# Kernel optimization log

Measured on AMD Instinct MI355X. Metric: run time of the kernel, lower is better.

Reference implementation:

```python
import jax, jax.numpy as jnp
import numpy as np

B, Q, KV = 8, 16, 2048
NQ, NK, NV, H = 512, 512, 512, 512

def setup_inputs() -> dict:
    key = jax.random.key(0)
    k = jax.random.split(key, 7)
    s = 0.02
    return {
        "query": jax.random.normal(k[0], (B, Q, NQ), jnp.float32),
        "keys": jax.random.normal(k[1], (B, KV, NK), jnp.float32),
        "values": jax.random.normal(k[2], (B, KV, NV), jnp.float32),
        "W_weight": jax.random.normal(k[3], (H, NQ + NK), jnp.float32) * s,
        "W_bias": jax.random.normal(k[4], (H,), jnp.float32) * s,
        "v_weight": jax.random.normal(k[5], (1, H), jnp.float32) * s,
        "v_bias": jax.random.normal(k[6], (1,), jnp.float32) * s,
    }

def reference(query, keys, values, W_weight, W_bias, v_weight, v_bias):
    # Split W over the concat axis: cat([query, keys]) @ W^T == query@Wq^T + keys@Wk^T
    Wq = W_weight[:, :NQ]   # [H, Nq]
    Wk = W_weight[:, NQ:]   # [H, Nk]
    q_part = jnp.einsum('bqn,hn->bqh', query, Wq)   # [B,Q,H]
    k_part = jnp.einsum('bkn,hn->bkh', keys, Wk)    # [B,KV,H]
    # broadcast-add -> [B,KV,Q,H], tanh, project to scalar energy
    energy = jnp.tanh(k_part[:, :, None, :] + q_part[:, None, :, :] + W_bias)
    e = jnp.einsum('bkqh,h->bkq', energy, v_weight[0]) + v_bias[0]  # [B,KV,Q]
    scores = jax.nn.softmax(e, axis=1)              # softmax over KV
    # output = (values^T @ scores)^T -> [B,Q,Nv]
    output = jnp.einsum('bkn,bkq->bqn', values, scores)
    return output
```

## Files before the change

### kernel.cpp

```cpp
#include <hip/hip_runtime.h>
#include <cstddef>

using bf16x8  = __attribute__((ext_vector_type(8))) short;
using short4v = __attribute__((ext_vector_type(4))) short;
using f32x4   = __attribute__((ext_vector_type(4))) float;
using ushort8 = __attribute__((ext_vector_type(8))) unsigned short;

#define GLL16(gp, lp) __builtin_amdgcn_global_load_lds( \
    (const __attribute__((address_space(1))) unsigned int*)(const void*)(gp), \
    (__attribute__((address_space(3))) unsigned int*)(void*)(lp), 16, 0, 0)

__device__ __forceinline__ float exp2_f(float x){ float r; asm("v_exp_f32 %0, %1" : "=v"(r) : "v"(x)); return r; }
__device__ __forceinline__ float rcp_f (float x){ float r; asm("v_rcp_f32 %0, %1" : "=v"(r) : "v"(x)); return r; }
__device__ __forceinline__ unsigned pk2(float lo, float hi){
  unsigned r; asm("v_cvt_pk_bf16_f32 %0, %1, %2" : "=v"(r) : "v"(lo), "v"(hi)); return r;
}
__device__ __forceinline__ unsigned short f2bf(float f){
  unsigned int u = __float_as_uint(f);
  u = u + 0x7FFFu + ((u >> 16) & 1u);
  return (unsigned short)(u >> 16);
}
__device__ __forceinline__ float bf2f(unsigned short s){
  return __uint_as_float(((unsigned int)s) << 16);
}

#define KEYS_N   8388608
#define WK_N     262144
#define CONV_BLOCKS 4224
#define SCALE_2LOG2E 2.885390081777927f

#define OFF_KEYS_BF   0u
#define OFF_WK_BF     16777216u
#define OFF_EQB       17301504u
#define OFF_EPART     17563648u
#define OFF_SC        21757952u

__global__ __launch_bounds__(256) void k_convert(
    const float* __restrict__ keys, const float* __restrict__ W,
    const float* __restrict__ query,
    unsigned short* __restrict__ keys_bf, unsigned short* __restrict__ wk_bf,
    float* __restrict__ eqb)
{
  __shared__ short qg[128*32 + 32*32];
  if (blockIdx.x >= CONV_BLOCKS) {
    const int nb = blockIdx.x - CONV_BLOCKS;
    const int n0 = nb * 32;
    const int tid = threadIdx.x;
    const int l = tid & 63, w = tid >> 6;
    short* A  = qg;
    short* Bs = qg + 4096;
    const int sub = tid >> 3;
    const int c4  = (tid & 7) * 4;
    const int wm = w & 1, wn = w >> 1;
    const int fr = l & 15, fg = l >> 4;

    f32x4 acc[4];
    #pragma unroll
    for (int i = 0; i < 4; ++i) acc[i] = (f32x4){0.f,0.f,0.f,0.f};

    for (int kt = 0; kt < 16; ++kt) {
      const int k0 = kt * 32;
      float4 a4[4];
      #pragma unroll
      for (int m = 0; m < 4; ++m)
        a4[m] = *(const float4*)(query + (size_t)(m * 32 + sub) * 512 + k0 + c4);
      const float4 b4 = *(const float4*)(W + (size_t)(n0 + sub) * 1024 + k0 + c4);
      __syncthreads();
      #pragma unroll
      for (int m = 0; m < 4; ++m) {
        const int row = m * 32 + sub;
        const int o = row * 32 + (((c4 >> 3) ^ ((row >> 1) & 3)) << 3) + (c4 & 7);
        *(uint2*)&A[o] = make_uint2(pk2(a4[m].x, a4[m].y), pk2(a4[m].z, a4[m].w));
      }
      {
        const int o = sub * 32 + (((c4 >> 3) ^ ((sub >> 1) & 3)) << 3) + (c4 & 7);
        *(uint2*)&Bs[o] = make_uint2(pk2(b4.x, b4.y), pk2(b4.z, b4.w));
      }
      __syncthreads();
      bf16x8 af[4], bfv;
      #pragma unroll
      for (int i = 0; i < 4; ++i) {
        const int ar = wm*64 + i*16 + fr;
        af[i] = *(const bf16x8*)&A[ar*32 + ((fg ^ ((ar>>1)&3)) << 3)];
      }
      const int br = wn*16 + fr;
      bfv = *(const bf16x8*)&Bs[br*32 + ((fg ^ ((br>>1)&3)) << 3)];
      #pragma unroll
      for (int i = 0; i < 4; ++i)
        acc[i] = __builtin_amdgcn_mfma_f32_16x16x32_bf16(af[i], bfv, acc[i], 0, 0, 0);
    }
    const int gh = n0 + wn*16 + fr;
    #pragma unroll
    for (int i = 0; i < 4; ++i)
      #pragma unroll
      for (int r = 0; r < 4; ++r) {
        const int gm = wm*64 + i*16 + fg*4 + r;
        eqb[gm * 512 + gh] = exp2_f(acc[i][r] * SCALE_2LOG2E);
      }
    return;
  }
  int idx = (blockIdx.x * 256 + threadIdx.x) * 8;
  const float* src;
  unsigned short* dst;
  if (idx < KEYS_N) { src = keys + idx; dst = keys_bf + idx; }
  else {
    int e = idx - KEYS_N;
    src = W + (size_t)(e >> 9) * 1024 + 512 + (e & 511);
    dst = wk_bf + e;
  }
  float4 a = *(const float4*)src;
  float4 b = *(const float4*)(src + 4);
  ushort8 o;
  o[0]=f2bf(a.x); o[1]=f2bf(a.y); o[2]=f2bf(a.z); o[3]=f2bf(a.w);
  o[4]=f2bf(b.x); o[5]=f2bf(b.y); o[6]=f2bf(b.z); o[7]=f2bf(b.w);
  *(ushort8*)dst = o;
}

struct FusedSM {
  union {
    struct { short A[8192]; short B[8192]; } g;
    unsigned short ekbf[128 * 128];
  } u;
  float eqs[16 * 128];
};

__global__ __launch_bounds__(256, 3) void k_fused(
    const unsigned short* __restrict__ keys_bf, const unsigned short* __restrict__ wk_bf,
    const float* __restrict__ w_bias, const float* __restrict__ eqb,
    const float* __restrict__ vw, float* __restrict__ e_part)
{
  __shared__ FusedSM sm;
  const int tid = threadIdx.x;
  const int l = tid & 63, w = tid >> 6;
  const int by = blockIdx.x;
  const int hc = blockIdx.y;
  const int h0 = hc * 128;
  const int b  = by >> 4;

  {
    const int q = tid >> 4, c0 = (tid & 15) * 8;
    const float* src = eqb + (size_t)(b * 16 + q) * 512 + h0 + c0;
    *(float4*)&sm.eqs[q * 128 + c0]     = *(const float4*)src;
    *(float4*)&sm.eqs[q * 128 + c0 + 4] = *(const float4*)(src + 4);
  }

  const unsigned short* Aptr = keys_bf + (size_t)by * 128 * 512;
  const unsigned short* Bptr = wk_bf + (size_t)h0 * 512;

  const int srow = w * 32 + (l >> 3);
  const int scol = ((l & 7) ^ (l >> 3)) * 8;
  const int wm = w >> 1, wn = w & 1;
  const int fr = l & 15, fg = l >> 4;
  const int axk = fr & 7;

  f32x4 acc[4][4];
  #pragma unroll
  for (int i = 0; i < 4; ++i)
    #pragma unroll
    for (int j = 0; j < 4; ++j) acc[i][j] = (f32x4){0.f,0.f,0.f,0.f};

  for (int kt = 0; kt < 8; ++kt) {
    const int k0 = kt * 64;
    #pragma unroll
    for (int r = 0; r < 4; ++r) {
      GLL16(Aptr + (srow + r * 8) * 512 + k0 + scol, &sm.u.g.A[w * 2048 + r * 512]);
      GLL16(Bptr + (srow + r * 8) * 512 + k0 + scol, &sm.u.g.B[w * 2048 + r * 512]);
    }
    __syncthreads();
    #pragma unroll
    for (int ks = 0; ks < 2; ++ks) {
      bf16x8 af[4], bfv[4];
      #pragma unroll
      for (int i = 0; i < 4; ++i) {
        af[i]  = *(const bf16x8*)&sm.u.g.A[(wm*64 + i*16 + fr) * 64 + ((ks*4 + fg) ^ axk) * 8];
        bfv[i] = *(const bf16x8*)&sm.u.g.B[(wn*64 + i*16 + fr) * 64 + ((ks*4 + fg) ^ axk) * 8];
      }
      #pragma unroll
      for (int i = 0; i < 4; ++i)
        #pragma unroll
        for (int j = 0; j < 4; ++j)
          acc[i][j] = __builtin_amdgcn_mfma_f32_16x16x32_bf16(af[i], bfv[j], acc[i][j], 0, 0, 0);
    }
    __syncthreads();
  }

  #pragma unroll
  for (int j = 0; j < 4; ++j) {
    const int col = wn*64 + j*16 + fr;
    const float bias = w_bias[h0 + col];
    const int chunk = col >> 3, coff = col & 7;
    #pragma unroll
    for (int i = 0; i < 4; ++i)
      #pragma unroll
      for (int r = 0; r < 4; ++r) {
        const int row = wm*64 + i*16 + fg*4 + r;
        const float ev = exp2_f((acc[i][j][r] + bias) * SCALE_2LOG2E);
        sm.u.ekbf[row * 128 + ((chunk ^ (fg*4 + r)) << 3) + coff] = f2bf(ev);
      }
  }
  const int g = l & 3, kl = l >> 2;
  float vv[32];
  #pragma unroll
  for (int s = 0; s < 4; ++s) {
    const float4 a0 = *(const float4*)(vw + h0 + s*32 + g*4);
    const float4 a1 = *(const float4*)(vw + h0 + s*32 + 16 + g*4);
    vv[s*8+0]=-2.f*a0.x; vv[s*8+1]=-2.f*a0.y; vv[s*8+2]=-2.f*a0.z; vv[s*8+3]=-2.f*a0.w;
    vv[s*8+4]=-2.f*a1.x; vv[s*8+5]=-2.f*a1.y; vv[s*8+6]=-2.f*a1.z; vv[s*8+7]=-2.f*a1.w;
  }
  __syncthreads();

  {
    const int lr0 = w * 32 + kl;
    const int lr1 = lr0 + 16;
    float ek0[32], ek1[32];
    #pragma unroll
    for (int s = 0; s < 4; ++s)
      #pragma unroll
      for (int hf = 0; hf < 2; ++hf) {
        const int ck = (4*s + 2*hf + (g >> 1)) ^ kl;
        const short4v v40 = *(const short4v*)&sm.u.ekbf[lr0 * 128 + (ck << 3) + (g & 1) * 4];
        const short4v v41 = *(const short4v*)&sm.u.ekbf[lr1 * 128 + (ck << 3) + (g & 1) * 4];
        #pragma unroll
        for (int u = 0; u < 4; ++u) {
          ek0[s*8 + hf*4 + u] = bf2f((unsigned short)v40[u]);
          ek1[s*8 + hf*4 + u] = bf2f((unsigned short)v41[u]);
        }
      }
    const size_t ep0 = (size_t)hc * 262144 + ((size_t)(by * 128 + lr0)) * 16;
    const size_t ep1 = (size_t)hc * 262144 + ((size_t)(by * 128 + lr1)) * 16;
    #pragma unroll 2
    for (int q = 0; q < 16; ++q) {
      float a00 = 0.f, a01 = 0.f, a10 = 0.f, a11 = 0.f;
      #pragma unroll
      for (int s = 0; s < 4; ++s) {
        const float* er = &sm.eqs[q * 128 + s * 32 + g * 4];
        const float4 E0 = *(const float4*)er;
        const float4 E1 = *(const float4*)(er + 16);
        a00 = fmaf(vv[s*8+0], rcp_f(fmaf(ek0[s*8+0], E0.x, 1.f)), a00);
        a01 = fmaf(vv[s*8+1], rcp_f(fmaf(ek0[s*8+1], E0.y, 1.f)), a01);
        a00 = fmaf(vv[s*8+2], rcp_f(fmaf(ek0[s*8+2], E0.z, 1.f)), a00);
        a01 = fmaf(vv[s*8+3], rcp_f(fmaf(ek0[s*8+3], E0.w, 1.f)), a01);
        a00 = fmaf(vv[s*8+4], rcp_f(fmaf(ek0[s*8+4], E1.x, 1.f)), a00);
        a01 = fmaf(vv[s*8+5], rcp_f(fmaf(ek0[s*8+5], E1.y, 1.f)), a01);
        a00 = fmaf(vv[s*8+6], rcp_f(fmaf(ek0[s*8+6], E1.z, 1.f)), a00);
        a01 = fmaf(vv[s*8+7], rcp_f(fmaf(ek0[s*8+7], E1.w, 1.f)), a01);
        a10 = fmaf(vv[s*8+0], rcp_f(fmaf(ek1[s*8+0], E0.x, 1.f)), a10);
        a11 = fmaf(vv[s*8+1], rcp_f(fmaf(ek1[s*8+1], E0.y, 1.f)), a11);
        a10 = fmaf(vv[s*8+2], rcp_f(fmaf(ek1[s*8+2], E0.z, 1.f)), a10);
        a11 = fmaf(vv[s*8+3], rcp_f(fmaf(ek1[s*8+3], E0.w, 1.f)), a11);
        a10 = fmaf(vv[s*8+4], rcp_f(fmaf(ek1[s*8+4], E1.x, 1.f)), a10);
        a11 = fmaf(vv[s*8+5], rcp_f(fmaf(ek1[s*8+5], E1.y, 1.f)), a11);
        a10 = fmaf(vv[s*8+6], rcp_f(fmaf(ek1[s*8+6], E1.z, 1.f)), a10);
        a11 = fmaf(vv[s*8+7], rcp_f(fmaf(ek1[s*8+7], E1.w, 1.f)), a11);
      }
      float r0 = a00 + a01;
      r0 += __shfl_xor(r0, 1, 64);
      r0 += __shfl_xor(r0, 2, 64);
      float r1 = a10 + a11;
      r1 += __shfl_xor(r1, 1, 64);
      r1 += __shfl_xor(r1, 2, 64);
      if (g == 0) { e_part[ep0 + q] = r0; e_part[ep1 + q] = r1; }
    }
  }
}

__global__ __launch_bounds__(256) void k_softmax(
    const float* __restrict__ e_part, float* __restrict__ sc)
{
  const int b = blockIdx.x >> 4, q = blockIdx.x & 15;
  const int base = b * 32768 + q;
  const int tid = threadIdx.x;
  __shared__ float redm[4], reds[4];

  float vals[8];
  float mx = -1e30f;
  #pragma unroll
  for (int i = 0; i < 8; ++i) {
    const int x = base + (tid + i * 256) * 16;
    vals[i] = (e_part[x] + e_part[x + 262144]) + (e_part[x + 524288] + e_part[x + 786432]);
    mx = fmaxf(mx, vals[i]);
  }
  #pragma unroll
  for (int msk = 1; msk < 64; msk <<= 1) mx = fmaxf(mx, __shfl_xor(mx, msk, 64));
  if ((tid & 63) == 0) redm[tid >> 6] = mx;
  __syncthreads();
  mx = fmaxf(fmaxf(redm[0], redm[1]), fmaxf(redm[2], redm[3]));

  float ex[8], sum = 0.f;
  #pragma unroll
  for (int i = 0; i < 8; ++i) { ex[i] = __expf(vals[i] - mx); sum += ex[i]; }
  #pragma unroll
  for (int msk = 1; msk < 64; msk <<= 1) sum += __shfl_xor(sum, msk, 64);
  if ((tid & 63) == 0) reds[tid >> 6] = sum;
  __syncthreads();
  sum = reds[0] + reds[1] + reds[2] + reds[3];
  const float r = 1.f / sum;
  #pragma unroll
  for (int i = 0; i < 8; ++i) sc[base + (tid + i * 256) * 16] = ex[i] * r;
}

__global__ __launch_bounds__(512) void k_pv(
    const float* __restrict__ values, const float* __restrict__ sc,
    float* __restrict__ out)
{
  __shared__ float lds[128 * 20];
  const int tid = threadIdx.x;
  const int nc = blockIdx.x & 31, b = blockIdx.x >> 5;
  const int n = tid & 15, kg = tid >> 4;
  const int l = tid & 63, w = tid >> 6;
  const int n0 = nc * 16;

  float acc[16];
  #pragma unroll
  for (int q = 0; q < 16; ++q) acc[q] = 0.f;

  for (int kc = 0; kc < 16; ++kc) {
    __syncthreads();
    {
      const float* ssrc = sc + (size_t)(b * 2048 + kc * 128) * 16;
      const int row = tid >> 2, c4 = (tid & 3) * 4;
      *(float4*)&lds[row * 20 + c4] = *(const float4*)&ssrc[row * 16 + c4];
    }
    __syncthreads();
    const float* vb = values + ((size_t)(b * 2048 + kc * 128 + kg * 4)) * 512 + n0 + n;
    #pragma unroll
    for (int k2 = 0; k2 < 4; ++k2) {
      const float v = vb[(size_t)k2 * 512];
      const float* sr = &lds[(kg * 4 + k2) * 20];
      #pragma unroll
      for (int qq = 0; qq < 4; ++qq) {
        const float4 s4 = *(const float4*)&sr[qq * 4];
        acc[qq*4+0] = fmaf(v, s4.x, acc[qq*4+0]);
        acc[qq*4+1] = fmaf(v, s4.y, acc[qq*4+1]);
        acc[qq*4+2] = fmaf(v, s4.z, acc[qq*4+2]);
        acc[qq*4+3] = fmaf(v, s4.w, acc[qq*4+3]);
      }
    }
  }
  #pragma unroll
  for (int q = 0; q < 16; ++q) {
    acc[q] += __shfl_xor(acc[q], 16, 64);
    acc[q] += __shfl_xor(acc[q], 32, 64);
  }
  __syncthreads();
  if (l < 16) {
    #pragma unroll
    for (int q = 0; q < 16; ++q) lds[w * 256 + q * 16 + l] = acc[q];
  }
  __syncthreads();
  if (tid < 256) {
    const int q = tid >> 4, nn = tid & 15;
    float s = 0.f;
    #pragma unroll
    for (int w2 = 0; w2 < 8; ++w2) s += lds[w2 * 256 + q * 16 + nn];
    out[((size_t)(b * 16 + q)) * 512 + n0 + nn] = s;
  }
}

extern "C" void kernel_launch(void* const* d_in, const int* in_sizes, int n_in,
                              void* d_out, int out_size, void* d_ws, size_t ws_size,
                              hipStream_t stream)
{
  const float* query  = (const float*)d_in[0];
  const float* keys   = (const float*)d_in[1];
  const float* values = (const float*)d_in[2];
  const float* W      = (const float*)d_in[3];
  const float* w_bias = (const float*)d_in[4];
  const float* vw     = (const float*)d_in[5];

  char* ws = (char*)d_ws;
  unsigned short* keys_bf = (unsigned short*)(ws + OFF_KEYS_BF);
  unsigned short* wk_bf   = (unsigned short*)(ws + OFF_WK_BF);
  float* eqb    = (float*)(ws + OFF_EQB);
  float* e_part = (float*)(ws + OFF_EPART);
  float* sc     = (float*)(ws + OFF_SC);

  hipLaunchKernelGGL(k_convert, dim3(CONV_BLOCKS + 16), dim3(256), 0, stream,
                     keys, W, query, keys_bf, wk_bf, eqb);
  hipLaunchKernelGGL(k_fused, dim3(128, 4), dim3(256), 0, stream,
                     keys_bf, wk_bf, w_bias, eqb, vw, e_part);
  hipLaunchKernelGGL(k_softmax, dim3(128), dim3(256), 0, stream, e_part, sc);
  hipLaunchKernelGGL(k_pv, dim3(256), dim3(512), 0, stream, values, sc, (float*)d_out);
}
```

Baseline: 87.52 us.

## Double-buffer k_fused GEMM tiles and prefetch query-GEMM loads in convert

The keys×Wk GEMM in k_fused now uses two LDS buffers. The next K-tile is issued with global_load_lds while the current one is computed, using explicit vmcnt waits and barriers. The small query GEMM blocks in k_convert are moved to the front of the grid so they start early, and their global loads are register-prefetched one iteration ahead. LDS use per block rises, so launch bounds drop from 3 to 2 blocks per CU, trading occupancy for overlap.

```diff
diff --git a/kernel.cpp b/kernel.cpp
--- a/kernel.cpp
+++ b/kernel.cpp
@@ -25,7 +25,7 @@
 }
 
 #define KEYS_N   8388608
-#define WK_N     262144
+#define QG_BLOCKS 16
 #define CONV_BLOCKS 4224
 #define SCALE_2LOG2E 2.885390081777927f
 
@@ -42,9 +42,8 @@
     float* __restrict__ eqb)
 {
   __shared__ short qg[128*32 + 32*32];
-  if (blockIdx.x >= CONV_BLOCKS) {
-    const int nb = blockIdx.x - CONV_BLOCKS;
-    const int n0 = nb * 32;
+  if (blockIdx.x < QG_BLOCKS) {
+    const int n0 = blockIdx.x * 32;
     const int tid = threadIdx.x;
     const int l = tid & 63, w = tid >> 6;
     short* A  = qg;
@@ -58,13 +57,20 @@
     #pragma unroll
     for (int i = 0; i < 4; ++i) acc[i] = (f32x4){0.f,0.f,0.f,0.f};
 
+    float4 a4[4], b4, a4n[4], b4n;
+    #pragma unroll
+    for (int m = 0; m < 4; ++m)
+      a4[m] = *(const float4*)(query + (size_t)(m * 32 + sub) * 512 + c4);
+    b4 = *(const float4*)(W + (size_t)(n0 + sub) * 1024 + c4);
+
     for (int kt = 0; kt < 16; ++kt) {
-      const int k0 = kt * 32;
-      float4 a4[4];
-      #pragma unroll
-      for (int m = 0; m < 4; ++m)
-        a4[m] = *(const float4*)(query + (size_t)(m * 32 + sub) * 512 + k0 + c4);
-      const float4 b4 = *(const float4*)(W + (size_t)(n0 + sub) * 1024 + k0 + c4);
+      if (kt < 15) {
+        const int k0 = (kt + 1) * 32;
+        #pragma unroll
+        for (int m = 0; m < 4; ++m)
+          a4n[m] = *(const float4*)(query + (size_t)(m * 32 + sub) * 512 + k0 + c4);
+        b4n = *(const float4*)(W + (size_t)(n0 + sub) * 1024 + k0 + c4);
+      }
       __syncthreads();
       #pragma unroll
       for (int m = 0; m < 4; ++m) {
@@ -88,6 +94,11 @@
       #pragma unroll
       for (int i = 0; i < 4; ++i)
         acc[i] = __builtin_amdgcn_mfma_f32_16x16x32_bf16(af[i], bfv, acc[i], 0, 0, 0);
+      if (kt < 15) {
+        #pragma unroll
+        for (int m = 0; m < 4; ++m) a4[m] = a4n[m];
+        b4 = b4n;
+      }
     }
     const int gh = n0 + wn*16 + fr;
     #pragma unroll
@@ -99,7 +110,7 @@
       }
     return;
   }
-  int idx = (blockIdx.x * 256 + threadIdx.x) * 8;
+  int idx = ((blockIdx.x - QG_BLOCKS) * 256 + threadIdx.x) * 8;
   const float* src;
   unsigned short* dst;
   if (idx < KEYS_N) { src = keys + idx; dst = keys_bf + idx; }
@@ -118,13 +129,13 @@
 
 struct FusedSM {
   union {
-    struct { short A[8192]; short B[8192]; } g;
+    struct { short A[2][8192]; short B[2][8192]; } g;
     unsigned short ekbf[128 * 128];
   } u;
   float eqs[16 * 128];
 };
 
-__global__ __launch_bounds__(256, 3) void k_fused(
+__global__ __launch_bounds__(256, 2) void k_fused(
     const unsigned short* __restrict__ keys_bf, const unsigned short* __restrict__ wk_bf,
     const float* __restrict__ w_bias, const float* __restrict__ eqb,
     const float* __restrict__ vw, float* __restrict__ e_part)
@@ -159,21 +170,22 @@
     #pragma unroll
     for (int j = 0; j < 4; ++j) acc[i][j] = (f32x4){0.f,0.f,0.f,0.f};
 
-  for (int kt = 0; kt < 8; ++kt) {
+  auto stage = [&](int buf, int kt) {
     const int k0 = kt * 64;
     #pragma unroll
     for (int r = 0; r < 4; ++r) {
-      GLL16(Aptr + (srow + r * 8) * 512 + k0 + scol, &sm.u.g.A[w * 2048 + r * 512]);
-      GLL16(Bptr + (srow + r * 8) * 512 + k0 + scol, &sm.u.g.B[w * 2048 + r * 512]);
-    }
-    __syncthreads();
+      GLL16(Aptr + (srow + r * 8) * 512 + k0 + scol, &sm.u.g.A[buf][w * 2048 + r * 512]);
+      GLL16(Bptr + (srow + r * 8) * 512 + k0 + scol, &sm.u.g.B[buf][w * 2048 + r * 512]);
+    }
+  };
+  auto compute = [&](int buf) {
     #pragma unroll
     for (int ks = 0; ks < 2; ++ks) {
       bf16x8 af[4], bfv[4];
       #pragma unroll
       for (int i = 0; i < 4; ++i) {
-        af[i]  = *(const bf16x8*)&sm.u.g.A[(wm*64 + i*16 + fr) * 64 + ((ks*4 + fg) ^ axk) * 8];
-        bfv[i] = *(const bf16x8*)&sm.u.g.B[(wn*64 + i*16 + fr) * 64 + ((ks*4 + fg) ^ axk) * 8];
+        af[i]  = *(const bf16x8*)&sm.u.g.A[buf][(wm*64 + i*16 + fr) * 64 + ((ks*4 + fg) ^ axk) * 8];
+        bfv[i] = *(const bf16x8*)&sm.u.g.B[buf][(wn*64 + i*16 + fr) * 64 + ((ks*4 + fg) ^ axk) * 8];
       }
       #pragma unroll
       for (int i = 0; i < 4; ++i)
@@ -181,7 +193,25 @@
         for (int j = 0; j < 4; ++j)
           acc[i][j] = __builtin_amdgcn_mfma_f32_16x16x32_bf16(af[i], bfv[j], acc[i][j], 0, 0, 0);
     }
-    __syncthreads();
+  };
+
+  stage(0, 0);
+  #pragma unroll 1
+  for (int kt = 0; kt < 8; ++kt) {
+    if (kt < 7) {
+      stage((kt + 1) & 1, kt + 1);
+      asm volatile("s_waitcnt vmcnt(8)" ::: "memory");
+    } else {
+      asm volatile("s_waitcnt vmcnt(0)" ::: "memory");
+    }
+    __builtin_amdgcn_sched_barrier(0);
+    __builtin_amdgcn_s_barrier();
+    __builtin_amdgcn_sched_barrier(0);
+    compute(kt & 1);
+    asm volatile("s_waitcnt lgkmcnt(0)" ::: "memory");
+    __builtin_amdgcn_sched_barrier(0);
+    __builtin_amdgcn_s_barrier();
+    __builtin_amdgcn_sched_barrier(0);
   }
 
   #pragma unroll
@@ -375,7 +405,7 @@
   float* e_part = (float*)(ws + OFF_EPART);
   float* sc     = (float*)(ws + OFF_SC);
 
-  hipLaunchKernelGGL(k_convert, dim3(CONV_BLOCKS + 16), dim3(256), 0, stream,
+  hipLaunchKernelGGL(k_convert, dim3(QG_BLOCKS + CONV_BLOCKS), dim3(256), 0, stream,
                      keys, W, query, keys_bf, wk_bf, eqb);
   hipLaunchKernelGGL(k_fused, dim3(128, 4), dim3(256), 0, stream,
                      keys_bf, wk_bf, w_bias, eqb, vw, e_part);
```

New measurement: 85.32 us. 2.5% less time.
